# Optimization experiments

Hardware: AMD Instinct MI355X
Metric: run time of the kernel (lower is better)

The kernel has to match this reference:

```python
import jax, jax.numpy as jnp
import numpy as np

WS = 8        # window_size
NH = 8        # num_heads
SHIFT = WS // 2  # cyclic shift amount (shift=True)
EPS = 1e-5


def _layernorm(x, g, b):
    m = x.mean(-1, keepdims=True)
    v = ((x - m) ** 2).mean(-1, keepdims=True)
    return (x - m) * jax.lax.rsqrt(v + EPS) * g + b


def setup_inputs() -> dict:
    key = jax.random.key(0)
    ks = jax.random.split(key, 6)
    B, C, H, W = 8, 256, 128, 128
    hidden = 4 * C
    return {
        "x": jax.random.normal(ks[0], (B, C, H, W), dtype=jnp.float32),
        "norm1_g": jnp.ones((C,), jnp.float32),
        "norm1_b": jnp.zeros((C,), jnp.float32),
        "w_qkv": 0.02 * jax.random.normal(ks[1], (C, 3 * C), dtype=jnp.float32),
        "b_qkv": jnp.zeros((3 * C,), jnp.float32),
        "w_proj": 0.02 * jax.random.normal(ks[2], (C, C), dtype=jnp.float32),
        "b_proj": jnp.zeros((C,), jnp.float32),
        "norm2_g": jnp.ones((C,), jnp.float32),
        "norm2_b": jnp.zeros((C,), jnp.float32),
        "w1": 0.02 * jax.random.normal(ks[3], (C, hidden), dtype=jnp.float32),
        "b1": jnp.zeros((hidden,), jnp.float32),
        "w2": 0.02 * jax.random.normal(ks[4], (hidden, C), dtype=jnp.float32),
        "b2": jnp.zeros((C,), jnp.float32),
    }


def reference(x, norm1_g, norm1_b, w_qkv, b_qkv, w_proj, b_proj,
              norm2_g, norm2_b, w1, b1, w2, b2):
    B, C, H, W = x.shape
    hd = C // NH
    scale = hd ** -0.5

    xh = jnp.transpose(x, (0, 2, 3, 1))          # B,H,W,C
    shortcut = xh
    y = _layernorm(xh, norm1_g, norm1_b)
    y = jnp.roll(y, (-SHIFT, -SHIFT), axis=(1, 2))  # cyclic shift

    # window partition -> (Bw, N, C), N = WS*WS
    y = y.reshape(B, H // WS, WS, W // WS, WS, C)
    y = y.transpose(0, 1, 3, 2, 4, 5).reshape(-1, WS * WS, C)
    Bw, N, _ = y.shape

    qkv = (y @ w_qkv + b_qkv).reshape(Bw, N, 3, NH, hd).transpose(2, 0, 3, 1, 4)
    q, k, v = qkv[0], qkv[1], qkv[2]             # each (Bw, NH, N, hd)
    att = jax.nn.softmax(jnp.einsum('bhnd,bhmd->bhnm', q, k) * scale, axis=-1)
    o = jnp.einsum('bhnm,bhmd->bhnd', att, v)
    o = o.transpose(0, 2, 1, 3).reshape(Bw, N, C) @ w_proj + b_proj

    # window reverse -> B,H,W,C
    y = o.reshape(B, H // WS, W // WS, WS, WS, C)
    y = y.transpose(0, 1, 3, 2, 4, 5).reshape(B, H, W, C)
    y = jnp.roll(y, (SHIFT, SHIFT), axis=(1, 2))  # reverse shift

    xh = y + shortcut                             # attention residual

    # MLP branch: computed in the original module but its output is DISCARDED
    # (original returns `x + shortcut` where shortcut == x, i.e. 2*x).
    h = _layernorm(xh, norm2_g, norm2_b)
    h = jax.nn.gelu(h @ w1 + b1, approximate=False) @ w2 + b2  # unused, faithful to source

    out = xh + xh                                 # replicates original `x + shortcut`
    return jnp.transpose(out, (0, 3, 1, 2))       # back to B,C,H,W
```

## Files before the change

### kernel.cpp

```cpp
#include <hip/hip_runtime.h>
#include <stdint.h>

#define SHIFT 4
#define EPS 1e-5f

#define B_ 8
#define C_ 256
#define H_ 128
#define W_ 128
#define HW_ (H_*W_)
#define NWIN 2048
#define NTOK (NWIN*64)

typedef unsigned short u16;
typedef float f32x4 __attribute__((ext_vector_type(4)));
typedef __bf16 bf16x8 __attribute__((ext_vector_type(8)));
typedef unsigned short u16x8 __attribute__((ext_vector_type(8)));

#define GLOAD16(gp, lp) __builtin_amdgcn_global_load_lds( \
    (const __attribute__((address_space(1))) uint32_t*)(gp), \
    (__attribute__((address_space(3))) uint32_t*)(lp), 16, 0, 0)

static __device__ __forceinline__ u16 f2bf(float f) {
    uint32_t u = __builtin_bit_cast(uint32_t, f);
    u = u + 0x7fffu + ((u >> 16) & 1u);
    return (u16)(u >> 16);
}
static __device__ __forceinline__ float bf2f(u16 u) {
    return __builtin_bit_cast(float, (uint32_t)u << 16);
}

__global__ __launch_bounds__(256) void k_prep_w(const float* __restrict__ wqkv,
                                                const float* __restrict__ wproj,
                                                u16* __restrict__ W2q, u16* __restrict__ W2pA) {
    int i = blockIdx.x * 256 + threadIdx.x;
    if (i < 48 * 8 * 64 * 8) {
        int e = i & 7, l = (i >> 3) & 63, kt = (i >> 9) & 7, jg = i >> 12;
        int col = jg * 16 + (l & 15);
        int k = kt * 32 + (l >> 4) * 8 + e;
        W2q[i] = f2bf(wqkv[k * 768 + col]);
    } else {
        int j = i - 48 * 8 * 64 * 8;
        int e = j & 7, l = (j >> 3) & 63, kt = (j >> 9) & 7, ig = j >> 12;
        int c = ig * 16 + (l & 15);
        int k = kt * 32 + (l >> 4) * 8 + e;
        W2pA[j] = f2bf(wproj[k * 256 + c]);
    }
}

__global__ __launch_bounds__(256) void k_ln_win(const float* __restrict__ x,
                                                const float* __restrict__ g,
                                                const float* __restrict__ beta,
                                                u16* __restrict__ ywin) {
    __shared__ u16 sv[256][130];
    __shared__ float ps[2][128];
    __shared__ float pss[2][128];
    __shared__ float mval[128];
    __shared__ float rval[128];
    int h = blockIdx.x;
    int b = blockIdx.y;
    int t = threadIdx.x;
    int p = t >> 7, w = t & 127;
    const float* xb = x + (size_t)b * C_ * HW_ + (size_t)h * W_;
    float s = 0.f, ss = 0.f;
    #pragma unroll 8
    for (int it = 0; it < 128; ++it) {
        int c = it * 2 + p;
        float v = xb[(size_t)c * HW_ + w];
        s += v; ss += v * v;
        sv[c][w] = f2bf(v);
    }
    ps[p][w] = s;
    pss[p][w] = ss;
    __syncthreads();
    if (t < 128) {
        float st = ps[0][t] + ps[1][t];
        float sst = pss[0][t] + pss[1][t];
        float m = st * (1.f / C_);
        float var = sst * (1.f / C_) - m * m;
        mval[t] = m;
        rval[t] = rsqrtf(var + EPS);
    }
    __syncthreads();
    int hp = (h - SHIFT) & 127;
    int wh = hp >> 3, r = hp & 7;
    int c = t;
    float gc = g[c], bc = beta[c];
    int winbase = (b * 16 + wh) * 16;
    #pragma unroll 4
    for (int wp = 0; wp < 128; ++wp) {
        int wsrc = (wp + SHIFT) & 127;
        float v = bf2f(sv[c][wsrc]);
        float yv = (v - mval[wsrc]) * rval[wsrc] * gc + bc;
        int row = (winbase + (wp >> 3)) * 64 + r * 8 + (wp & 7);
        ywin[(size_t)row * C_ + c] = f2bf(yv);
    }
}

__global__ __launch_bounds__(512) void k_fused(const u16* __restrict__ ywin,
                                               const u16* __restrict__ W2q,
                                               const u16* __restrict__ W2pA,
                                               const float* __restrict__ bqkv,
                                               const float* __restrict__ bproj,
                                               const float* __restrict__ x,
                                               float* __restrict__ out) {
    extern __shared__ __align__(16) char smem[];
    u16* Y  = (u16*)smem;
    u16* QK = (u16*)(smem + 32768);
    u16* VT = (u16*)(smem + 114688);
    u16* O  = (u16*)(smem + 114688);

    int bid = blockIdx.x;
    int win = (bid & 7) * 256 + (bid >> 3);
    int b = win >> 8, wh = (win >> 4) & 15, ww = win & 15;

    int t = threadIdx.x;
    int wave = t >> 6, lane = t & 63;
    int lr = lane & 15, lk = lane >> 4;

    {
        const u16* base = ywin + (size_t)win * 64 * 256;
        #pragma unroll
        for (int q = 0; q < 4; ++q) {
            int g = wave * 256 + q * 64 + lane;
            int n = g >> 5, pc = g & 31;
            int sc = pc ^ (n & 31);
            GLOAD16(base + n * 256 + sc * 8, smem + wave * 4096 + q * 1024);
        }
    }
    __syncthreads();

    {
        f32x4 acc[4][6];
        #pragma unroll
        for (int i = 0; i < 4; ++i)
            #pragma unroll
            for (int j = 0; j < 6; ++j) acc[i][j] = (f32x4){0.f,0.f,0.f,0.f};
        #pragma unroll
        for (int kt = 0; kt < 8; ++kt) {
            bf16x8 af[4], bf[6];
            #pragma unroll
            for (int i = 0; i < 4; ++i) {
                int n = i * 16 + lr;
                int pc = (kt * 4 + lk) ^ (n & 31);
                af[i] = __builtin_bit_cast(bf16x8, *(const u16x8*)(&Y[n * 256 + pc * 8]));
            }
            #pragma unroll
            for (int j = 0; j < 6; ++j) {
                int jg = wave * 6 + j;
                bf[j] = __builtin_bit_cast(bf16x8,
                    *(const u16x8*)(W2q + (((size_t)(jg * 8 + kt)) << 9) + (lane << 3)));
            }
            #pragma unroll
            for (int i = 0; i < 4; ++i)
                #pragma unroll
                for (int j = 0; j < 6; ++j)
                    acc[i][j] = __builtin_amdgcn_mfma_f32_16x16x32_bf16(af[i], bf[j], acc[i][j], 0, 0, 0);
        }
        #pragma unroll
        for (int j = 0; j < 6; ++j) {
            int col = wave * 96 + j * 16 + lr;
            int which = col >> 8, rem = col & 255;
            int head = rem >> 5, d = rem & 31;
            float bi = bqkv[col];
            #pragma unroll
            for (int i = 0; i < 4; ++i)
                #pragma unroll
                for (int rg = 0; rg < 4; ++rg) {
                    int n = i * 16 + lk * 4 + rg;
                    u16 v = f2bf(acc[i][j][rg] + bi);
                    if (which < 2) QK[which * 20480 + head * 2560 + n * 40 + d] = v;
                    else           VT[head * 2304 + d * 72 + n] = v;
                }
        }
    }
    __syncthreads();

    f32x4 oacc[4][2];
    {
        const u16* qb = QK + wave * 2560;
        const u16* kb = QK + 20480 + wave * 2560;
        f32x4 sacc[4][4];
        #pragma unroll
        for (int i = 0; i < 4; ++i)
            #pragma unroll
            for (int j = 0; j < 4; ++j) sacc[i][j] = (f32x4){0.f,0.f,0.f,0.f};
        bf16x8 qf[4], kf[4];
        #pragma unroll
        for (int i = 0; i < 4; ++i)
            qf[i] = __builtin_bit_cast(bf16x8, *(const u16x8*)(qb + (i * 16 + lr) * 40 + lk * 8));
        #pragma unroll
        for (int j = 0; j < 4; ++j)
            kf[j] = __builtin_bit_cast(bf16x8, *(const u16x8*)(kb + (j * 16 + lr) * 40 + lk * 8));
        #pragma unroll
        for (int i = 0; i < 4; ++i)
            #pragma unroll
            for (int j = 0; j < 4; ++j)
                sacc[i][j] = __builtin_amdgcn_mfma_f32_16x16x32_bf16(qf[i], kf[j], sacc[i][j], 0, 0, 0);
        __syncthreads();

        u16* Pw = (u16*)(smem + wave * 9216);
        const float scale = 0.17677669529663687f;
        #pragma unroll
        for (int i = 0; i < 4; ++i) {
            #pragma unroll
            for (int rg = 0; rg < 4; ++rg) {
                float s0 = sacc[i][0][rg] * scale, s1 = sacc[i][1][rg] * scale;
                float s2 = sacc[i][2][rg] * scale, s3 = sacc[i][3][rg] * scale;
                float mx = fmaxf(fmaxf(s0, s1), fmaxf(s2, s3));
                mx = fmaxf(mx, __shfl_xor(mx, 1));
                mx = fmaxf(mx, __shfl_xor(mx, 2));
                mx = fmaxf(mx, __shfl_xor(mx, 4));
                mx = fmaxf(mx, __shfl_xor(mx, 8));
                float p0 = __expf(s0 - mx), p1 = __expf(s1 - mx);
                float p2 = __expf(s2 - mx), p3 = __expf(s3 - mx);
                float sm = p0 + p1 + p2 + p3;
                sm += __shfl_xor(sm, 1);
                sm += __shfl_xor(sm, 2);
                sm += __shfl_xor(sm, 4);
                sm += __shfl_xor(sm, 8);
                float rs = 1.f / sm;
                int row = i * 16 + lk * 4 + rg;
                Pw[row * 72 + 0 * 16 + lr] = f2bf(p0 * rs);
                Pw[row * 72 + 1 * 16 + lr] = f2bf(p1 * rs);
                Pw[row * 72 + 2 * 16 + lr] = f2bf(p2 * rs);
                Pw[row * 72 + 3 * 16 + lr] = f2bf(p3 * rs);
            }
        }
        #pragma unroll
        for (int i = 0; i < 4; ++i)
            #pragma unroll
            for (int j = 0; j < 2; ++j) oacc[i][j] = (f32x4){0.f,0.f,0.f,0.f};
        const u16* vtw = VT + wave * 2304;
        #pragma unroll
        for (int ks = 0; ks < 2; ++ks) {
            bf16x8 pf[4], vf[2];
            #pragma unroll
            for (int i = 0; i < 4; ++i)
                pf[i] = __builtin_bit_cast(bf16x8, *(const u16x8*)(&Pw[(i * 16 + lr) * 72 + ks * 32 + lk * 8]));
            #pragma unroll
            for (int j = 0; j < 2; ++j)
                vf[j] = __builtin_bit_cast(bf16x8, *(const u16x8*)(vtw + (j * 16 + lr) * 72 + ks * 32 + lk * 8));
            #pragma unroll
            for (int i = 0; i < 4; ++i)
                #pragma unroll
                for (int j = 0; j < 2; ++j)
                    oacc[i][j] = __builtin_amdgcn_mfma_f32_16x16x32_bf16(pf[i], vf[j], oacc[i][j], 0, 0, 0);
        }
    }
    __syncthreads();

    #pragma unroll
    for (int i = 0; i < 4; ++i)
        #pragma unroll
        for (int j = 0; j < 2; ++j)
            #pragma unroll
            for (int rg = 0; rg < 4; ++rg) {
                int n = i * 16 + lk * 4 + rg;
                O[n * 280 + wave * 32 + j * 16 + lr] = f2bf(oacc[i][j][rg]);
            }
    __syncthreads();

    f32x4 acc2[2][4];
    #pragma unroll
    for (int i = 0; i < 2; ++i)
        #pragma unroll
        for (int j = 0; j < 4; ++j) acc2[i][j] = (f32x4){0.f,0.f,0.f,0.f};
    #pragma unroll
    for (int kt = 0; kt < 8; ++kt) {
        bf16x8 af[2], bo[4];
        #pragma unroll
        for (int i = 0; i < 2; ++i) {
            int ig = wave * 2 + i;
            af[i] = __builtin_bit_cast(bf16x8,
                *(const u16x8*)(W2pA + (((size_t)(ig * 8 + kt)) << 9) + (lane << 3)));
        }
        #pragma unroll
        for (int j = 0; j < 4; ++j)
            bo[j] = __builtin_bit_cast(bf16x8, *(const u16x8*)(&O[(j * 16 + lr) * 280 + kt * 32 + lk * 8]));
        #pragma unroll
        for (int i = 0; i < 2; ++i)
            #pragma unroll
            for (int j = 0; j < 4; ++j)
                acc2[i][j] = __builtin_amdgcn_mfma_f32_16x16x32_bf16(af[i], bo[j], acc2[i][j], 0, 0, 0);
    }

    {
        int hbase = wh * 8 + SHIFT;
        int wbase = ww * 8 + SHIFT;
        #pragma unroll
        for (int i = 0; i < 2; ++i)
            #pragma unroll
            for (int rg = 0; rg < 4; ++rg) {
                int c = wave * 32 + i * 16 + lk * 4 + rg;
                float bi = bproj[c];
                size_t cb = ((size_t)(b * 256 + c)) << 14;
                #pragma unroll
                for (int j = 0; j < 4; ++j) {
                    int token = j * 16 + lr;
                    int r = token >> 3, s = token & 7;
                    int hs = (hbase + r) & 127;
                    int wc = (wbase + s) & 127;
                    size_t oi = cb + hs * 128 + wc;
                    out[oi] = 2.f * (acc2[i][j][rg] + bi + x[oi]);
                }
            }
    }
}

extern "C" void kernel_launch(void* const* d_in, const int* in_sizes, int n_in,
                              void* d_out, int out_size, void* d_ws, size_t ws_size,
                              hipStream_t stream) {
    const float* x     = (const float*)d_in[0];
    const float* g1    = (const float*)d_in[1];
    const float* bb1   = (const float*)d_in[2];
    const float* wqkv  = (const float*)d_in[3];
    const float* bqkv  = (const float*)d_in[4];
    const float* wproj = (const float*)d_in[5];
    const float* bproj = (const float*)d_in[6];
    float* out = (float*)d_out;

    char* ws = (char*)d_ws;
    u16* W2q  = (u16*)ws;
    u16* W2pA = (u16*)(ws + 393216);
    u16* ywin = (u16*)(ws + (1ull << 20));

    static const int LDS_BYTES = 151552;
    hipFuncSetAttribute((const void*)k_fused,
                        hipFuncAttributeMaxDynamicSharedMemorySize, LDS_BYTES);

    k_prep_w<<<1024, 256, 0, stream>>>(wqkv, wproj, W2q, W2pA);
    k_ln_win<<<dim3(128, 8), 256, 0, stream>>>(x, g1, bb1, ywin);
    k_fused<<<NWIN, 512, LDS_BYTES, stream>>>(ywin, W2q, W2pA, bqkv, bproj, x, out);
}
```

Measured before the change: 260.9 us.

## Restructure fused window attention per-head with MFMA-fragment ywin layout and smaller LDS

The LayerNorm kernel now writes the windowed activations directly in MFMA A-fragment order, so the fused kernel loads Q/K/V operands from global memory instead of staging the whole window in LDS. Each wave computes its own head's Q, K and V, runs the softmax, and keeps the probabilities in registers, using a small per-wave LDS scratch. This removes most block-wide barriers and cuts LDS from about 148KB to 80KB so more blocks can be resident per CU (launch bounds set to 4). In exchange, every wave re-reads the activation fragments from global/L2 twice (once for QK, once for V), which adds memory traffic.

```diff
diff --git a/kernel.cpp b/kernel.cpp
--- a/kernel.cpp
+++ b/kernel.cpp
@@ -10,16 +10,12 @@
 #define W_ 128
 #define HW_ (H_*W_)
 #define NWIN 2048
-#define NTOK (NWIN*64)
 
 typedef unsigned short u16;
 typedef float f32x4 __attribute__((ext_vector_type(4)));
 typedef __bf16 bf16x8 __attribute__((ext_vector_type(8)));
 typedef unsigned short u16x8 __attribute__((ext_vector_type(8)));
-
-#define GLOAD16(gp, lp) __builtin_amdgcn_global_load_lds( \
-    (const __attribute__((address_space(1))) uint32_t*)(gp), \
-    (__attribute__((address_space(3))) uint32_t*)(lp), 16, 0, 0)
+typedef unsigned short u16x4 __attribute__((ext_vector_type(4)));
 
 static __device__ __forceinline__ u16 f2bf(float f) {
     uint32_t u = __builtin_bit_cast(uint32_t, f);
@@ -51,7 +47,7 @@
 __global__ __launch_bounds__(256) void k_ln_win(const float* __restrict__ x,
                                                 const float* __restrict__ g,
                                                 const float* __restrict__ beta,
-                                                u16* __restrict__ ywin) {
+                                                u16* __restrict__ ywin2) {
     __shared__ u16 sv[256][130];
     __shared__ float ps[2][128];
     __shared__ float pss[2][128];
@@ -84,205 +80,235 @@
     __syncthreads();
     int hp = (h - SHIFT) & 127;
     int wh = hp >> 3, r = hp & 7;
+    int i_f = r >> 1;
+    int lrb = (r & 1) * 8;
     int c = t;
     float gc = g[c], bc = beta[c];
-    int winbase = (b * 16 + wh) * 16;
+    int kt = c >> 5, lk2 = (c >> 3) & 3, e = c & 7;
+    int winrow = (b * 16 + wh) * 16;
+    u16* dst = ywin2 + (size_t)winrow * 16384 + kt * 2048 + i_f * 512 + lk2 * 128 + lrb * 8 + e;
     #pragma unroll 4
     for (int wp = 0; wp < 128; ++wp) {
         int wsrc = (wp + SHIFT) & 127;
         float v = bf2f(sv[c][wsrc]);
         float yv = (v - mval[wsrc]) * rval[wsrc] * gc + bc;
-        int row = (winbase + (wp >> 3)) * 64 + r * 8 + (wp & 7);
-        ywin[(size_t)row * C_ + c] = f2bf(yv);
-    }
-}
-
-__global__ __launch_bounds__(512) void k_fused(const u16* __restrict__ ywin,
-                                               const u16* __restrict__ W2q,
-                                               const u16* __restrict__ W2pA,
-                                               const float* __restrict__ bqkv,
-                                               const float* __restrict__ bproj,
-                                               const float* __restrict__ x,
-                                               float* __restrict__ out) {
+        dst[(size_t)(wp >> 3) * 16384 + (wp & 7) * 8] = f2bf(yv);
+    }
+}
+
+__global__ __launch_bounds__(512, 4) void k_fused(const u16* __restrict__ ywin2,
+                                                  const u16* __restrict__ W2q,
+                                                  const u16* __restrict__ W2pA,
+                                                  const float* __restrict__ bqkv,
+                                                  const float* __restrict__ bproj,
+                                                  const float* __restrict__ x,
+                                                  float* __restrict__ out) {
     extern __shared__ __align__(16) char smem[];
-    u16* Y  = (u16*)smem;
-    u16* QK = (u16*)(smem + 32768);
-    u16* VT = (u16*)(smem + 114688);
-    u16* O  = (u16*)(smem + 114688);
-
     int bid = blockIdx.x;
     int win = (bid & 7) * 256 + (bid >> 3);
     int b = win >> 8, wh = (win >> 4) & 15, ww = win & 15;
-
     int t = threadIdx.x;
     int wave = t >> 6, lane = t & 63;
     int lr = lane & 15, lk = lane >> 4;
-
+    int hd = wave;
+
+    u16* WR = (u16*)smem + wave * 5120;
+    u16* Q  = WR;
+    u16* K  = WR + 2560;
+    u16* VT = WR;
+    u16* Ph = WR + 2560;
+    u16* O  = (u16*)smem;
+
+    const u16* afp = ywin2 + (size_t)win * 16384;
+
+    f32x4 acc[4][4];
+    #pragma unroll
+    for (int i = 0; i < 4; ++i)
+        #pragma unroll
+        for (int j = 0; j < 4; ++j) acc[i][j] = (f32x4){0.f,0.f,0.f,0.f};
+    #pragma unroll 2
+    for (int kt = 0; kt < 8; ++kt) {
+        bf16x8 af[4], bq[4];
+        #pragma unroll
+        for (int i = 0; i < 4; ++i)
+            af[i] = __builtin_bit_cast(bf16x8, *(const u16x8*)(afp + kt * 2048 + i * 512 + lane * 8));
+        #pragma unroll
+        for (int jl = 0; jl < 4; ++jl) {
+            int jg = (jl >> 1) * 16 + 2 * hd + (jl & 1);
+            bq[jl] = __builtin_bit_cast(bf16x8, *(const u16x8*)(W2q + ((size_t)(jg * 8 + kt)) * 512 + lane * 8));
+        }
+        #pragma unroll
+        for (int i = 0; i < 4; ++i)
+            #pragma unroll
+            for (int jl = 0; jl < 4; ++jl)
+                acc[i][jl] = __builtin_amdgcn_mfma_f32_16x16x32_bf16(af[i], bq[jl], acc[i][jl], 0, 0, 0);
+    }
+    #pragma unroll
+    for (int jl = 0; jl < 4; ++jl) {
+        int which = jl >> 1;
+        int d = (jl & 1) * 16 + lr;
+        float bi = bqkv[which * 256 + hd * 32 + d];
+        u16* dst = which ? K : Q;
+        #pragma unroll
+        for (int i = 0; i < 4; ++i)
+            #pragma unroll
+            for (int rg = 0; rg < 4; ++rg)
+                dst[(i * 16 + lk * 4 + rg) * 40 + d] = f2bf(acc[i][jl][rg] + bi);
+    }
+    bf16x8 qf[4], kf[4];
+    #pragma unroll
+    for (int i = 0; i < 4; ++i)
+        qf[i] = __builtin_bit_cast(bf16x8, *(const u16x8*)(&Q[(i * 16 + lr) * 40 + lk * 8]));
+    #pragma unroll
+    for (int j = 0; j < 4; ++j)
+        kf[j] = __builtin_bit_cast(bf16x8, *(const u16x8*)(&K[(j * 16 + lr) * 40 + lk * 8]));
+    f32x4 s[4][4];
+    #pragma unroll
+    for (int i = 0; i < 4; ++i)
+        #pragma unroll
+        for (int j = 0; j < 4; ++j) s[i][j] = (f32x4){0.f,0.f,0.f,0.f};
+    #pragma unroll
+    for (int i = 0; i < 4; ++i)
+        #pragma unroll
+        for (int j = 0; j < 4; ++j)
+            s[i][j] = __builtin_amdgcn_mfma_f32_16x16x32_bf16(qf[i], kf[j], s[i][j], 0, 0, 0);
+
+    const float scale = 0.17677669529663687f;
+    #pragma unroll
+    for (int i = 0; i < 4; ++i) {
+        #pragma unroll
+        for (int rg = 0; rg < 4; ++rg) {
+            float s0 = s[i][0][rg] * scale, s1 = s[i][1][rg] * scale;
+            float s2 = s[i][2][rg] * scale, s3 = s[i][3][rg] * scale;
+            float mx = fmaxf(fmaxf(s0, s1), fmaxf(s2, s3));
+            mx = fmaxf(mx, __shfl_xor(mx, 1));
+            mx = fmaxf(mx, __shfl_xor(mx, 2));
+            mx = fmaxf(mx, __shfl_xor(mx, 4));
+            mx = fmaxf(mx, __shfl_xor(mx, 8));
+            float p0 = __expf(s0 - mx), p1 = __expf(s1 - mx);
+            float p2 = __expf(s2 - mx), p3 = __expf(s3 - mx);
+            float sm = p0 + p1 + p2 + p3;
+            sm += __shfl_xor(sm, 1);
+            sm += __shfl_xor(sm, 2);
+            sm += __shfl_xor(sm, 4);
+            sm += __shfl_xor(sm, 8);
+            float rs = 1.f / sm;
+            s[i][0][rg] = p0 * rs; s[i][1][rg] = p1 * rs;
+            s[i][2][rg] = p2 * rs; s[i][3][rg] = p3 * rs;
+        }
+    }
+    #pragma unroll
+    for (int j2 = 0; j2 < 2; ++j2)
+        #pragma unroll
+        for (int i = 0; i < 4; ++i)
+            #pragma unroll
+            for (int rg = 0; rg < 4; ++rg)
+                Ph[(i * 16 + lk * 4 + rg) * 40 + j2 * 16 + lr] = f2bf(s[i][j2][rg]);
+
+    f32x4 av[4][2];
+    #pragma unroll
+    for (int i = 0; i < 4; ++i)
+        #pragma unroll
+        for (int j = 0; j < 2; ++j) av[i][j] = (f32x4){0.f,0.f,0.f,0.f};
+    #pragma unroll 2
+    for (int kt = 0; kt < 8; ++kt) {
+        bf16x8 af[4], bv[2];
+        #pragma unroll
+        for (int i = 0; i < 4; ++i)
+            af[i] = __builtin_bit_cast(bf16x8, *(const u16x8*)(afp + kt * 2048 + i * 512 + lane * 8));
+        #pragma unroll
+        for (int jl = 0; jl < 2; ++jl) {
+            int jg = 32 + 2 * hd + jl;
+            bv[jl] = __builtin_bit_cast(bf16x8, *(const u16x8*)(W2q + ((size_t)(jg * 8 + kt)) * 512 + lane * 8));
+        }
+        #pragma unroll
+        for (int i = 0; i < 4; ++i)
+            #pragma unroll
+            for (int jl = 0; jl < 2; ++jl)
+                av[i][jl] = __builtin_amdgcn_mfma_f32_16x16x32_bf16(af[i], bv[jl], av[i][jl], 0, 0, 0);
+    }
+    #pragma unroll
+    for (int jl = 0; jl < 2; ++jl) {
+        float bi = bqkv[512 + hd * 32 + jl * 16 + lr];
+        #pragma unroll
+        for (int i = 0; i < 4; ++i) {
+            u16x4 pk;
+            #pragma unroll
+            for (int rg = 0; rg < 4; ++rg) pk[rg] = f2bf(av[i][jl][rg] + bi);
+            *(u16x4*)(&VT[(jl * 16 + lr) * 72 + i * 16 + lk * 4]) = pk;
+        }
+    }
+    f32x4 oacc[4][2];
+    #pragma unroll
+    for (int i = 0; i < 4; ++i)
+        #pragma unroll
+        for (int j = 0; j < 2; ++j) oacc[i][j] = (f32x4){0.f,0.f,0.f,0.f};
     {
-        const u16* base = ywin + (size_t)win * 64 * 256;
-        #pragma unroll
-        for (int q = 0; q < 4; ++q) {
-            int g = wave * 256 + q * 64 + lane;
-            int n = g >> 5, pc = g & 31;
-            int sc = pc ^ (n & 31);
-            GLOAD16(base + n * 256 + sc * 8, smem + wave * 4096 + q * 1024);
-        }
-    }
+        bf16x8 pf[4], vf[2];
+        #pragma unroll
+        for (int i = 0; i < 4; ++i)
+            pf[i] = __builtin_bit_cast(bf16x8, *(const u16x8*)(&Ph[(i * 16 + lr) * 40 + lk * 8]));
+        #pragma unroll
+        for (int j = 0; j < 2; ++j)
+            vf[j] = __builtin_bit_cast(bf16x8, *(const u16x8*)(&VT[(j * 16 + lr) * 72 + lk * 8]));
+        #pragma unroll
+        for (int i = 0; i < 4; ++i)
+            #pragma unroll
+            for (int j = 0; j < 2; ++j)
+                oacc[i][j] = __builtin_amdgcn_mfma_f32_16x16x32_bf16(pf[i], vf[j], oacc[i][j], 0, 0, 0);
+    }
+    #pragma unroll
+    for (int j2 = 2; j2 < 4; ++j2)
+        #pragma unroll
+        for (int i = 0; i < 4; ++i)
+            #pragma unroll
+            for (int rg = 0; rg < 4; ++rg)
+                Ph[(i * 16 + lk * 4 + rg) * 40 + (j2 & 1) * 16 + lr] = f2bf(s[i][j2][rg]);
+    {
+        bf16x8 pf[4], vf[2];
+        #pragma unroll
+        for (int i = 0; i < 4; ++i)
+            pf[i] = __builtin_bit_cast(bf16x8, *(const u16x8*)(&Ph[(i * 16 + lr) * 40 + lk * 8]));
+        #pragma unroll
+        for (int j = 0; j < 2; ++j)
+            vf[j] = __builtin_bit_cast(bf16x8, *(const u16x8*)(&VT[(j * 16 + lr) * 72 + 32 + lk * 8]));
+        #pragma unroll
+        for (int i = 0; i < 4; ++i)
+            #pragma unroll
+            for (int j = 0; j < 2; ++j)
+                oacc[i][j] = __builtin_amdgcn_mfma_f32_16x16x32_bf16(pf[i], vf[j], oacc[i][j], 0, 0, 0);
+    }
+
     __syncthreads();
-
-    {
-        f32x4 acc[4][6];
-        #pragma unroll
-        for (int i = 0; i < 4; ++i)
-            #pragma unroll
-            for (int j = 0; j < 6; ++j) acc[i][j] = (f32x4){0.f,0.f,0.f,0.f};
-        #pragma unroll
-        for (int kt = 0; kt < 8; ++kt) {
-            bf16x8 af[4], bf[6];
-            #pragma unroll
-            for (int i = 0; i < 4; ++i) {
-                int n = i * 16 + lr;
-                int pc = (kt * 4 + lk) ^ (n & 31);
-                af[i] = __builtin_bit_cast(bf16x8, *(const u16x8*)(&Y[n * 256 + pc * 8]));
-            }
-            #pragma unroll
-            for (int j = 0; j < 6; ++j) {
-                int jg = wave * 6 + j;
-                bf[j] = __builtin_bit_cast(bf16x8,
-                    *(const u16x8*)(W2q + (((size_t)(jg * 8 + kt)) << 9) + (lane << 3)));
-            }
-            #pragma unroll
-            for (int i = 0; i < 4; ++i)
-                #pragma unroll
-                for (int j = 0; j < 6; ++j)
-                    acc[i][j] = __builtin_amdgcn_mfma_f32_16x16x32_bf16(af[i], bf[j], acc[i][j], 0, 0, 0);
-        }
-        #pragma unroll
-        for (int j = 0; j < 6; ++j) {
-            int col = wave * 96 + j * 16 + lr;
-            int which = col >> 8, rem = col & 255;
-            int head = rem >> 5, d = rem & 31;
-            float bi = bqkv[col];
-            #pragma unroll
-            for (int i = 0; i < 4; ++i)
-                #pragma unroll
-                for (int rg = 0; rg < 4; ++rg) {
-                    int n = i * 16 + lk * 4 + rg;
-                    u16 v = f2bf(acc[i][j][rg] + bi);
-                    if (which < 2) QK[which * 20480 + head * 2560 + n * 40 + d] = v;
-                    else           VT[head * 2304 + d * 72 + n] = v;
-                }
-        }
-    }
+    #pragma unroll
+    for (int i = 0; i < 4; ++i)
+        #pragma unroll
+        for (int j = 0; j < 2; ++j)
+            #pragma unroll
+            for (int rg = 0; rg < 4; ++rg)
+                O[(i * 16 + lk * 4 + rg) * 280 + hd * 32 + j * 16 + lr] = f2bf(oacc[i][j][rg]);
     __syncthreads();
 
-    f32x4 oacc[4][2];
-    {
-        const u16* qb = QK + wave * 2560;
-        const u16* kb = QK + 20480 + wave * 2560;
-        f32x4 sacc[4][4];
-        #pragma unroll
-        for (int i = 0; i < 4; ++i)
-            #pragma unroll
-            for (int j = 0; j < 4; ++j) sacc[i][j] = (f32x4){0.f,0.f,0.f,0.f};
-        bf16x8 qf[4], kf[4];
-        #pragma unroll
-        for (int i = 0; i < 4; ++i)
-            qf[i] = __builtin_bit_cast(bf16x8, *(const u16x8*)(qb + (i * 16 + lr) * 40 + lk * 8));
-        #pragma unroll
-        for (int j = 0; j < 4; ++j)
-            kf[j] = __builtin_bit_cast(bf16x8, *(const u16x8*)(kb + (j * 16 + lr) * 40 + lk * 8));
-        #pragma unroll
-        for (int i = 0; i < 4; ++i)
-            #pragma unroll
-            for (int j = 0; j < 4; ++j)
-                sacc[i][j] = __builtin_amdgcn_mfma_f32_16x16x32_bf16(qf[i], kf[j], sacc[i][j], 0, 0, 0);
-        __syncthreads();
-
-        u16* Pw = (u16*)(smem + wave * 9216);
-        const float scale = 0.17677669529663687f;
-        #pragma unroll
-        for (int i = 0; i < 4; ++i) {
-            #pragma unroll
-            for (int rg = 0; rg < 4; ++rg) {
-                float s0 = sacc[i][0][rg] * scale, s1 = sacc[i][1][rg] * scale;
-                float s2 = sacc[i][2][rg] * scale, s3 = sacc[i][3][rg] * scale;
-                float mx = fmaxf(fmaxf(s0, s1), fmaxf(s2, s3));
-                mx = fmaxf(mx, __shfl_xor(mx, 1));
-                mx = fmaxf(mx, __shfl_xor(mx, 2));
-                mx = fmaxf(mx, __shfl_xor(mx, 4));
-                mx = fmaxf(mx, __shfl_xor(mx, 8));
-                float p0 = __expf(s0 - mx), p1 = __expf(s1 - mx);
-                float p2 = __expf(s2 - mx), p3 = __expf(s3 - mx);
-                float sm = p0 + p1 + p2 + p3;
-                sm += __shfl_xor(sm, 1);
-                sm += __shfl_xor(sm, 2);
-                sm += __shfl_xor(sm, 4);
-                sm += __shfl_xor(sm, 8);
-                float rs = 1.f / sm;
-                int row = i * 16 + lk * 4 + rg;
-                Pw[row * 72 + 0 * 16 + lr] = f2bf(p0 * rs);
-                Pw[row * 72 + 1 * 16 + lr] = f2bf(p1 * rs);
-                Pw[row * 72 + 2 * 16 + lr] = f2bf(p2 * rs);
-                Pw[row * 72 + 3 * 16 + lr] = f2bf(p3 * rs);
-            }
-        }
-        #pragma unroll
-        for (int i = 0; i < 4; ++i)
-            #pragma unroll
-            for (int j = 0; j < 2; ++j) oacc[i][j] = (f32x4){0.f,0.f,0.f,0.f};
-        const u16* vtw = VT + wave * 2304;
-        #pragma unroll
-        for (int ks = 0; ks < 2; ++ks) {
-            bf16x8 pf[4], vf[2];
-            #pragma unroll
-            for (int i = 0; i < 4; ++i)
-                pf[i] = __builtin_bit_cast(bf16x8, *(const u16x8*)(&Pw[(i * 16 + lr) * 72 + ks * 32 + lk * 8]));
-            #pragma unroll
-            for (int j = 0; j < 2; ++j)
-                vf[j] = __builtin_bit_cast(bf16x8, *(const u16x8*)(vtw + (j * 16 + lr) * 72 + ks * 32 + lk * 8));
-            #pragma unroll
-            for (int i = 0; i < 4; ++i)
-                #pragma unroll
-                for (int j = 0; j < 2; ++j)
-                    oacc[i][j] = __builtin_amdgcn_mfma_f32_16x16x32_bf16(pf[i], vf[j], oacc[i][j], 0, 0, 0);
-        }
-    }
-    __syncthreads();
-
-    #pragma unroll
-    for (int i = 0; i < 4; ++i)
-        #pragma unroll
-        for (int j = 0; j < 2; ++j)
-            #pragma unroll
-            for (int rg = 0; rg < 4; ++rg) {
-                int n = i * 16 + lk * 4 + rg;
-                O[n * 280 + wave * 32 + j * 16 + lr] = f2bf(oacc[i][j][rg]);
-            }
-    __syncthreads();
-
-    f32x4 acc2[2][4];
+    f32x4 c2[2][4];
     #pragma unroll
     for (int i = 0; i < 2; ++i)
         #pragma unroll
-        for (int j = 0; j < 4; ++j) acc2[i][j] = (f32x4){0.f,0.f,0.f,0.f};
-    #pragma unroll
+        for (int j = 0; j < 4; ++j) c2[i][j] = (f32x4){0.f,0.f,0.f,0.f};
+    #pragma unroll 2
     for (int kt = 0; kt < 8; ++kt) {
-        bf16x8 af[2], bo[4];
-        #pragma unroll
-        for (int i = 0; i < 2; ++i) {
-            int ig = wave * 2 + i;
-            af[i] = __builtin_bit_cast(bf16x8,
-                *(const u16x8*)(W2pA + (((size_t)(ig * 8 + kt)) << 9) + (lane << 3)));
-        }
+        bf16x8 a2[2], bo[4];
+        #pragma unroll
+        for (int i2 = 0; i2 < 2; ++i2)
+            a2[i2] = __builtin_bit_cast(bf16x8,
+                *(const u16x8*)(W2pA + ((size_t)((wave * 2 + i2) * 8 + kt)) * 512 + lane * 8));
         #pragma unroll
         for (int j = 0; j < 4; ++j)
             bo[j] = __builtin_bit_cast(bf16x8, *(const u16x8*)(&O[(j * 16 + lr) * 280 + kt * 32 + lk * 8]));
         #pragma unroll
-        for (int i = 0; i < 2; ++i)
+        for (int i2 = 0; i2 < 2; ++i2)
             #pragma unroll
             for (int j = 0; j < 4; ++j)
-                acc2[i][j] = __builtin_amdgcn_mfma_f32_16x16x32_bf16(af[i], bo[j], acc2[i][j], 0, 0, 0);
+                c2[i2][j] = __builtin_amdgcn_mfma_f32_16x16x32_bf16(a2[i2], bo[j], c2[i2][j], 0, 0, 0);
     }
 
     {
@@ -298,11 +324,11 @@
                 #pragma unroll
                 for (int j = 0; j < 4; ++j) {
                     int token = j * 16 + lr;
-                    int r = token >> 3, s = token & 7;
+                    int r = token >> 3, sgm = token & 7;
                     int hs = (hbase + r) & 127;
-                    int wc = (wbase + s) & 127;
+                    int wc = (wbase + sgm) & 127;
                     size_t oi = cb + hs * 128 + wc;
-                    out[oi] = 2.f * (acc2[i][j][rg] + bi + x[oi]);
+                    out[oi] = 2.f * (c2[i][j][rg] + bi + x[oi]);
                 }
             }
     }
@@ -323,13 +349,13 @@
     char* ws = (char*)d_ws;
     u16* W2q  = (u16*)ws;
     u16* W2pA = (u16*)(ws + 393216);
-    u16* ywin = (u16*)(ws + (1ull << 20));
-
-    static const int LDS_BYTES = 151552;
+    u16* ywin2 = (u16*)(ws + (1ull << 20));
+
+    static const int LDS_BYTES = 81920;
     hipFuncSetAttribute((const void*)k_fused,
                         hipFuncAttributeMaxDynamicSharedMemorySize, LDS_BYTES);
 
     k_prep_w<<<1024, 256, 0, stream>>>(wqkv, wproj, W2q, W2pA);
-    k_ln_win<<<dim3(128, 8), 256, 0, stream>>>(x, g1, bb1, ywin);
-    k_fused<<<NWIN, 512, LDS_BYTES, stream>>>(ywin, W2q, W2pA, bqkv, bproj, x, out);
-}
+    k_ln_win<<<dim3(128, 8), 256, 0, stream>>>(x, g1, bb1, ywin2);
+    k_fused<<<NWIN, 512, LDS_BYTES, stream>>>(ywin2, W2q, W2pA, bqkv, bproj, x, out);
+}
```

Result: faster. 243.8 us (median of 3 runs) (-6.5%).
